# Kernel optimization log

Measured on AMD Instinct MI355X. Metric: run time of the kernel, lower is better.

The kernel has to match this reference:

```python
import jax, jax.numpy as jnp
import numpy as np

NUM_HEADS = 16


def setup_inputs() -> dict:
    key = jax.random.key(0)
    k1, k2, k3 = jax.random.split(key, 3)
    x = jax.random.normal(k1, (2, 2048, 1024), dtype=jnp.float32)
    w_qkv = jax.random.normal(k2, (3072, 1024), dtype=jnp.float32) * 0.02
    b_qkv = jax.random.normal(k3, (3072,), dtype=jnp.float32) * 0.02
    return {"x": x, "w_qkv": w_qkv, "b_qkv": b_qkv}


def reference(x, w_qkv, b_qkv):
    b, s, _ = x.shape
    d_model = w_qkv.shape[0] // 3
    head_dim = d_model // NUM_HEADS
    # fused QKV projection (torch Linear: x @ W^T + b)
    qkv = x @ w_qkv.T + b_qkv                      # [b, s, 3*d_model]
    qkv = qkv.reshape(b, s, NUM_HEADS, 3 * head_dim)
    qkv = jnp.transpose(qkv, (0, 2, 1, 3))          # [b, h, s, 3*hd]
    q, k, v = jnp.split(qkv, 3, axis=-1)            # each [b, h, s, hd]
    scale = 1.0 / np.sqrt(head_dim).astype(np.float32)
    scores = jnp.einsum("bhqd,bhkd->bhqk", q, k) * scale
    attn = jax.nn.softmax(scores, axis=-1)
    values = jnp.einsum("bhqk,bhkd->bhqd", attn, v)  # [b, h, s, hd]
    # Faithful to source: reshape WITHOUT permuting heads back (head-interleaved)
    return values.reshape(b, s, d_model)
```

## Files before the change

### kernel.cpp

```cpp
#include <hip/hip_runtime.h>
#include <cstdint>

typedef unsigned short ushort_t;

#define M_ROWS 4096
#define N_COLS 3072
#define K_DIM  1024
#define S_LEN  2048
#define NHEADS 16
#define HDIM   64
#define QSCALE 0.1803368801111204f

typedef __bf16 bf16_t;
typedef bf16_t  bf16x8  __attribute__((ext_vector_type(8)));
typedef short   shortx4 __attribute__((ext_vector_type(4)));
typedef float   floatx4 __attribute__((ext_vector_type(4)));
typedef ushort_t ushortx4 __attribute__((ext_vector_type(4)));

union U32x2S4 { unsigned u[2]; shortx4 s; };

__device__ __forceinline__ unsigned short f2bf(float f) {
  unsigned u = __float_as_uint(f);
  u += 0x7FFFu + ((u >> 16) & 1u);
  return (unsigned short)(u >> 16);
}

__device__ __forceinline__ unsigned pkbf(float a, float b) {
  unsigned ua = __float_as_uint(a) + 0x8000u;
  unsigned ub = __float_as_uint(b) + 0x8000u;
  return __builtin_amdgcn_perm(ub, ua, 0x07060302u);
}

__device__ __forceinline__ float fexp2(float x) {
#if __has_builtin(__builtin_amdgcn_exp2f)
  return __builtin_amdgcn_exp2f(x);
#else
  float r; asm volatile("v_exp_f32 %0, %1\n\ts_nop 1" : "=v"(r) : "v"(x)); return r;
#endif
}

__device__ __forceinline__ void gload_lds16(const void* g, void* l) {
  __builtin_amdgcn_global_load_lds(
      (const __attribute__((address_space(1))) unsigned int*)g,
      (__attribute__((address_space(3))) unsigned int*)l,
      16, 0, 0);
}

__global__ __launch_bounds__(256) void cvt_bf16_kernel(
    const float* __restrict__ x, const float* __restrict__ w,
    ushort_t* __restrict__ Xb, ushort_t* __restrict__ Wb) {
  const int NX4 = (M_ROWS * K_DIM) / 4;
  int i = blockIdx.x * 256 + threadIdx.x;
  const float4* src;
  ushort_t* dst;
  int idx;
  if (i < NX4) { src = (const float4*)x; dst = Xb; idx = i; }
  else         { src = (const float4*)w; dst = Wb; idx = i - NX4; }
  float4 v = src[idx];
  ushort4 o;
  o.x = f2bf(v.x); o.y = f2bf(v.y); o.z = f2bf(v.z); o.w = f2bf(v.w);
  ((ushort4*)dst)[idx] = o;
}

__global__ __launch_bounds__(256) void qkv_gemm_kernel(
    const ushort_t* __restrict__ Xb, const ushort_t* __restrict__ Wb,
    const float* __restrict__ bias,
    ushort_t* __restrict__ Qb, ushort_t* __restrict__ Kb, ushort_t* __restrict__ Vb) {
  __shared__ ushort_t As[128 * 64];
  __shared__ ushort_t Bs[128 * 64];
  const int tid = threadIdx.x;
  const int l = tid & 63, w = tid >> 6;
  const int quad = l >> 4, lj = l & 15;
  const int m0 = blockIdx.y * 128, n0 = blockIdx.x * 128;
  const int wm = (w & 1) * 64, wn = (w >> 1) * 64;

  floatx4 acc[4][4] = {};

  const int srow = w * 32 + (l >> 3);
  const int scol = ((l & 7) ^ (l >> 3)) * 8;
  const ushort_t* gA = Xb + (size_t)(m0 + srow) * K_DIM + scol;
  const ushort_t* gB = Wb + (size_t)(n0 + srow) * K_DIM + scol;
  ushort_t* lA = As + (w * 32) * 64;
  ushort_t* lB = Bs + (w * 32) * 64;

  const int swr = lj & 7;

  for (int k0 = 0; k0 < K_DIM; k0 += 64) {
    __syncthreads();
#pragma unroll
    for (int c = 0; c < 4; ++c) {
      gload_lds16(gA + (size_t)(c * 8) * K_DIM + k0, lA + c * 8 * 64);
      gload_lds16(gB + (size_t)(c * 8) * K_DIM + k0, lB + c * 8 * 64);
    }
    __syncthreads();
#pragma unroll
    for (int kk = 0; kk < 2; ++kk) {
      const int ch = ((kk * 4 + quad) ^ swr) * 8;
      bf16x8 xF[4], wF[4];
#pragma unroll
      for (int j = 0; j < 4; ++j)
        xF[j] = *(const bf16x8*)(As + (wm + j * 16 + lj) * 64 + ch);
#pragma unroll
      for (int i = 0; i < 4; ++i)
        wF[i] = *(const bf16x8*)(Bs + (wn + i * 16 + lj) * 64 + ch);
#pragma unroll
      for (int i = 0; i < 4; ++i)
#pragma unroll
        for (int j = 0; j < 4; ++j)
          acc[i][j] = __builtin_amdgcn_mfma_f32_16x16x32_bf16(wF[i], xF[j], acc[i][j], 0, 0, 0);
    }
  }

  const int nseg = (n0 + wn) >> 6;
  const int h = nseg / 3;
  const int r = nseg - h * 3;
  ushort_t* dst = (r == 0) ? Qb : (r == 1) ? Kb : Vb;
  const float scl = (r == 0) ? QSCALE : 1.0f;
  const size_t hbase = (size_t)h * S_LEN * HDIM;

#pragma unroll
  for (int i = 0; i < 4; ++i) {
    const int d0 = i * 16 + quad * 4;
    const float4 bv = *(const float4*)(bias + n0 + wn + d0);
#pragma unroll
    for (int j = 0; j < 4; ++j) {
      const float v0 = (acc[i][j][0] + bv.x) * scl;
      const float v1 = (acc[i][j][1] + bv.y) * scl;
      const float v2 = (acc[i][j][2] + bv.z) * scl;
      const float v3 = (acc[i][j][3] + bv.w) * scl;
      uint2 pk;
      pk.x = pkbf(v0, v1);
      pk.y = pkbf(v2, v3);
      const int m = m0 + wm + j * 16 + lj;
      const int bi = m >> 11;
      const int si = m & 2047;
      *(uint2*)(dst + hbase + ((size_t)bi * NHEADS * S_LEN + si) * HDIM + d0) = pk;
    }
  }
}

__global__ __launch_bounds__(512, 4) void attn_kernel(
    const ushort_t* __restrict__ Qb, const ushort_t* __restrict__ Kb,
    const ushort_t* __restrict__ Vb, float* __restrict__ out) {
  __shared__ ushort_t Ks[128 * 64];
  __shared__ ushort_t Vs[64 * 140];
  const int tid = threadIdx.x;
  const int l = tid & 63, w = tid >> 6;
  const int quad = l >> 4, lj = l & 15;
  const int bh = blockIdx.x >> 4;
  const int qt = blockIdx.x & 15;
  const int q0 = qt * 128 + w * 16;
  const size_t headoff = (size_t)bh * S_LEN * HDIM;

  bf16x8 qF[2];
#pragma unroll
  for (int kk = 0; kk < 2; ++kk)
    qF[kk] = *(const bf16x8*)(Qb + headoff + (size_t)(q0 + lj) * HDIM +
                              kk * 32 + quad * 8);

  floatx4 accO[4] = {};
  float l_run = 0.f;

  const int kr = tid >> 3;
  const int kc = ((tid & 7) ^ (kr & 7)) * 8;
  const ushort_t* gK = Kb + headoff + (size_t)kr * HDIM + kc;
  ushort_t* lK = Ks + tid * 8;

  const int dq = tid & 15;
  const int spw = tid >> 4;
  const ushort_t* gV = Vb + headoff + dq * 4;
  unsigned* Vs32 = (unsigned*)Vs;
  const int swz = (dq >> 2) << 1;

  const int swk = lj & 7;

  for (int kb = 0; kb < 16; ++kb) {
    const int kv0 = kb * 128;
    __syncthreads();
#pragma unroll
    for (int c = 0; c < 2; ++c)
      gload_lds16(gK + (size_t)(kv0 + c * 64) * HDIM, lK + c * 64 * 64);
#pragma unroll
    for (int R = 0; R < 2; ++R) {
      const int sp = R * 32 + spw;
      const ushort_t* g = gV + (size_t)(kv0 + 2 * sp) * HDIM;
      const uint2 v0 = *(const uint2*)g;
      const uint2 v1 = *(const uint2*)(g + HDIM);
      unsigned o0 = __builtin_amdgcn_perm(v1.x, v0.x, 0x05040100u);
      unsigned o1 = __builtin_amdgcn_perm(v1.x, v0.x, 0x07060302u);
      unsigned o2 = __builtin_amdgcn_perm(v1.y, v0.y, 0x05040100u);
      unsigned o3 = __builtin_amdgcn_perm(v1.y, v0.y, 0x07060302u);
      const int sp2 = sp ^ swz;
      Vs32[(4 * dq + 0) * 70 + sp2] = o0;
      Vs32[(4 * dq + 1) * 70 + sp2] = o1;
      Vs32[(4 * dq + 2) * 70 + sp2] = o2;
      Vs32[(4 * dq + 3) * 70 + sp2] = o3;
    }
    __syncthreads();

    floatx4 accST[8];
#pragma unroll
    for (int c = 0; c < 8; ++c) {
      const ushort_t* krow = Ks + (c * 16 + lj) * 64;
      bf16x8 kF0 = *(const bf16x8*)(krow + ((quad ^ swk) * 8));
      bf16x8 kF1 = *(const bf16x8*)(krow + (((quad ^ swk) ^ 4) * 8));
      floatx4 z = {0.f, 0.f, 0.f, 0.f};
      z = __builtin_amdgcn_mfma_f32_16x16x32_bf16(kF0, qF[0], z, 0, 0, 0);
      accST[c] = __builtin_amdgcn_mfma_f32_16x16x32_bf16(kF1, qF[1], z, 0, 0, 0);
    }

    shortx4 aP[8];
    float lsum = 0.f;
#pragma unroll
    for (int c = 0; c < 8; ++c) {
      float p0 = fexp2(accST[c][0]);
      float p1 = fexp2(accST[c][1]);
      float p2 = fexp2(accST[c][2]);
      float p3 = fexp2(accST[c][3]);
      lsum += (p0 + p1) + (p2 + p3);
      U32x2S4 t;
      t.u[0] = pkbf(p0, p1);
      t.u[1] = pkbf(p2, p3);
      aP[c] = t.s;
    }
    l_run += lsum;

#pragma unroll
    for (int dt = 0; dt < 4; ++dt) {
      const ushort_t* vp = Vs + (dt * 16 + lj) * 140 + (quad ^ dt) * 4;
#pragma unroll
      for (int c = 0; c < 8; ++c) {
        shortx4 vF = *(const shortx4*)(vp + c * 16);
        accO[dt] = __builtin_amdgcn_mfma_f32_16x16x16bf16_1k(aP[c], vF, accO[dt], 0, 0, 0);
      }
    }
  }

  {
    float ls = l_run;
    ls += __shfl_xor(ls, 16, 64);
    ls += __shfl_xor(ls, 32, 64);
    const float inv = 1.0f / ls;
    const int sbase = (l & 48) | (quad * 4);
    float iv[4];
    iv[0] = __shfl(inv, sbase + 0, 64);
    iv[1] = __shfl(inv, sbase + 1, 64);
    iv[2] = __shfl(inv, sbase + 2, 64);
    iv[3] = __shfl(inv, sbase + 3, 64);
#pragma unroll
    for (int dt = 0; dt < 4; ++dt) {
#pragma unroll
      for (int rg = 0; rg < 4; ++rg) {
        const int q = q0 + quad * 4 + rg;
        out[headoff + (size_t)q * HDIM + dt * 16 + lj] = accO[dt][rg] * iv[rg];
      }
    }
  }
}

extern "C" void kernel_launch(void* const* d_in, const int* in_sizes, int n_in,
                              void* d_out, int out_size, void* d_ws, size_t ws_size,
                              hipStream_t stream) {
  (void)in_sizes; (void)n_in; (void)out_size; (void)ws_size;
  const float* x  = (const float*)d_in[0];
  const float* wq = (const float*)d_in[1];
  const float* bq = (const float*)d_in[2];
  float* out = (float*)d_out;

  char* ws = (char*)d_ws;
  ushort_t* Qb = (ushort_t*)(ws);
  ushort_t* Kb = (ushort_t*)(ws + 8388608);
  ushort_t* Vb = (ushort_t*)(ws + 16777216);
  ushort_t* Xb = (ushort_t*)(ws + 25165824);
  ushort_t* Wb = (ushort_t*)(ws + 33554432);

  cvt_bf16_kernel<<<7168, 256, 0, stream>>>(x, wq, Xb, Wb);
  qkv_gemm_kernel<<<dim3(N_COLS / 128, M_ROWS / 128), 256, 0, stream>>>(Xb, Wb, bq, Qb, Kb, Vb);
  attn_kernel<<<512, 512, 0, stream>>>(Qb, Kb, Vb, out);
}
```

Measured before the change: 171.3 us.

## Switch attention to 32x32 MFMA tiles with four waves per block

The attention kernel now uses 32x32x16 and 32x32x8 bf16 MFMAs, so each wave owns 32 query rows instead of 16. The block drops from 8 waves to 4 with the same 128 queries per block, and each thread loads more of the K/V tile. Processing each 32-key chunk immediately (scores, exp, PV) keeps fewer score registers live. The aim is fewer MFMA issues and fewer LDS fragment reads per FLOP, at the cost of fewer waves to hide latency and new lane-to-row mappings and swizzles that must match exactly.

```diff
diff --git a/kernel.cpp b/kernel.cpp
--- a/kernel.cpp
+++ b/kernel.cpp
@@ -15,6 +15,7 @@
 typedef bf16_t  bf16x8  __attribute__((ext_vector_type(8)));
 typedef short   shortx4 __attribute__((ext_vector_type(4)));
 typedef float   floatx4 __attribute__((ext_vector_type(4)));
+typedef float   floatx16 __attribute__((ext_vector_type(16)));
 typedef ushort_t ushortx4 __attribute__((ext_vector_type(4)));
 
 union U32x2S4 { unsigned u[2]; shortx4 s; };
@@ -139,26 +140,26 @@
   }
 }
 
-__global__ __launch_bounds__(512, 4) void attn_kernel(
+__global__ __launch_bounds__(256, 4) void attn_kernel(
     const ushort_t* __restrict__ Qb, const ushort_t* __restrict__ Kb,
     const ushort_t* __restrict__ Vb, float* __restrict__ out) {
   __shared__ ushort_t Ks[128 * 64];
   __shared__ ushort_t Vs[64 * 140];
   const int tid = threadIdx.x;
   const int l = tid & 63, w = tid >> 6;
-  const int quad = l >> 4, lj = l & 15;
+  const int dl = l & 31, h = l >> 5;
   const int bh = blockIdx.x >> 4;
   const int qt = blockIdx.x & 15;
-  const int q0 = qt * 128 + w * 16;
+  const int q0 = qt * 128 + w * 32;
   const size_t headoff = (size_t)bh * S_LEN * HDIM;
 
-  bf16x8 qF[2];
-#pragma unroll
-  for (int kk = 0; kk < 2; ++kk)
-    qF[kk] = *(const bf16x8*)(Qb + headoff + (size_t)(q0 + lj) * HDIM +
-                              kk * 32 + quad * 8);
-
-  floatx4 accO[4] = {};
+  bf16x8 qF[4];
+#pragma unroll
+  for (int t = 0; t < 4; ++t)
+    qF[t] = *(const bf16x8*)(Qb + headoff + (size_t)(q0 + dl) * HDIM +
+                             t * 16 + h * 8);
+
+  floatx16 accO[2] = {};
   float l_run = 0.f;
 
   const int kr = tid >> 3;
@@ -170,19 +171,17 @@
   const int spw = tid >> 4;
   const ushort_t* gV = Vb + headoff + dq * 4;
   unsigned* Vs32 = (unsigned*)Vs;
-  const int swz = (dq >> 2) << 1;
-
-  const int swk = lj & 7;
+  const int swzw = (dq >> 2) << 1;
 
   for (int kb = 0; kb < 16; ++kb) {
     const int kv0 = kb * 128;
     __syncthreads();
 #pragma unroll
-    for (int c = 0; c < 2; ++c)
-      gload_lds16(gK + (size_t)(kv0 + c * 64) * HDIM, lK + c * 64 * 64);
-#pragma unroll
-    for (int R = 0; R < 2; ++R) {
-      const int sp = R * 32 + spw;
+    for (int c = 0; c < 4; ++c)
+      gload_lds16(gK + (size_t)(kv0 + c * 32) * HDIM, lK + c * 32 * 64);
+#pragma unroll
+    for (int R = 0; R < 4; ++R) {
+      const int sp = R * 16 + spw;
       const ushort_t* g = gV + (size_t)(kv0 + 2 * sp) * HDIM;
       const uint2 v0 = *(const uint2*)g;
       const uint2 v1 = *(const uint2*)(g + HDIM);
@@ -190,7 +189,7 @@
       unsigned o1 = __builtin_amdgcn_perm(v1.x, v0.x, 0x07060302u);
       unsigned o2 = __builtin_amdgcn_perm(v1.y, v0.y, 0x05040100u);
       unsigned o3 = __builtin_amdgcn_perm(v1.y, v0.y, 0x07060302u);
-      const int sp2 = sp ^ swz;
+      const int sp2 = sp ^ swzw;
       Vs32[(4 * dq + 0) * 70 + sp2] = o0;
       Vs32[(4 * dq + 1) * 70 + sp2] = o1;
       Vs32[(4 * dq + 2) * 70 + sp2] = o2;
@@ -198,62 +197,58 @@
     }
     __syncthreads();
 
-    floatx4 accST[8];
-#pragma unroll
-    for (int c = 0; c < 8; ++c) {
-      const ushort_t* krow = Ks + (c * 16 + lj) * 64;
-      bf16x8 kF0 = *(const bf16x8*)(krow + ((quad ^ swk) * 8));
-      bf16x8 kF1 = *(const bf16x8*)(krow + (((quad ^ swk) ^ 4) * 8));
-      floatx4 z = {0.f, 0.f, 0.f, 0.f};
-      z = __builtin_amdgcn_mfma_f32_16x16x32_bf16(kF0, qF[0], z, 0, 0, 0);
-      accST[c] = __builtin_amdgcn_mfma_f32_16x16x32_bf16(kF1, qF[1], z, 0, 0, 0);
-    }
-
-    shortx4 aP[8];
-    float lsum = 0.f;
-#pragma unroll
-    for (int c = 0; c < 8; ++c) {
-      float p0 = fexp2(accST[c][0]);
-      float p1 = fexp2(accST[c][1]);
-      float p2 = fexp2(accST[c][2]);
-      float p3 = fexp2(accST[c][3]);
-      lsum += (p0 + p1) + (p2 + p3);
-      U32x2S4 t;
-      t.u[0] = pkbf(p0, p1);
-      t.u[1] = pkbf(p2, p3);
-      aP[c] = t.s;
-    }
-    l_run += lsum;
-
-#pragma unroll
-    for (int dt = 0; dt < 4; ++dt) {
-      const ushort_t* vp = Vs + (dt * 16 + lj) * 140 + (quad ^ dt) * 4;
-#pragma unroll
-      for (int c = 0; c < 8; ++c) {
-        shortx4 vF = *(const shortx4*)(vp + c * 16);
-        accO[dt] = __builtin_amdgcn_mfma_f32_16x16x16bf16_1k(aP[c], vF, accO[dt], 0, 0, 0);
+#pragma unroll
+    for (int c = 0; c < 4; ++c) {
+      const ushort_t* krow = Ks + (c * 32 + dl) * 64;
+      floatx16 s = {};
+#pragma unroll
+      for (int t = 0; t < 4; ++t) {
+        const int chunk = (t * 2 + h) ^ (dl & 7);
+        bf16x8 kF = *(const bf16x8*)(krow + chunk * 8);
+        s = __builtin_amdgcn_mfma_f32_32x32x16_bf16(kF, qF[t], s, 0, 0, 0);
       }
+
+      shortx4 aPt[4];
+      float lsum = 0.f;
+#pragma unroll
+      for (int c2 = 0; c2 < 4; ++c2) {
+        float p0 = fexp2(s[4 * c2 + 0]);
+        float p1 = fexp2(s[4 * c2 + 1]);
+        float p2 = fexp2(s[4 * c2 + 2]);
+        float p3 = fexp2(s[4 * c2 + 3]);
+        lsum += (p0 + p1) + (p2 + p3);
+        U32x2S4 tpk;
+        tpk.u[0] = pkbf(p0, p1);
+        tpk.u[1] = pkbf(p2, p3);
+        aPt[c2] = tpk.s;
+      }
+      l_run += lsum;
+
+#pragma unroll
+      for (int dt = 0; dt < 2; ++dt) {
+        const int d = dt * 32 + dl;
+        const int rsw = (d >> 4) << 1;
+        const ushort_t* vrow = Vs + d * 140;
+#pragma unroll
+        for (int c2 = 0; c2 < 4; ++c2) {
+          const int col = (c * 16 + c2 * 4 + h * 2) ^ rsw;
+          shortx4 vF = *(const shortx4*)(vrow + 2 * col);
+          accO[dt] = __builtin_amdgcn_mfma_f32_32x32x8bf16_1k(aPt[c2], vF, accO[dt], 0, 0, 0);
+        }
+      }
     }
   }
 
   {
-    float ls = l_run;
-    ls += __shfl_xor(ls, 16, 64);
-    ls += __shfl_xor(ls, 32, 64);
+    float ls = l_run + __shfl_xor(l_run, 32, 64);
     const float inv = 1.0f / ls;
-    const int sbase = (l & 48) | (quad * 4);
-    float iv[4];
-    iv[0] = __shfl(inv, sbase + 0, 64);
-    iv[1] = __shfl(inv, sbase + 1, 64);
-    iv[2] = __shfl(inv, sbase + 2, 64);
-    iv[3] = __shfl(inv, sbase + 3, 64);
-#pragma unroll
-    for (int dt = 0; dt < 4; ++dt) {
-#pragma unroll
-      for (int rg = 0; rg < 4; ++rg) {
-        const int q = q0 + quad * 4 + rg;
-        out[headoff + (size_t)q * HDIM + dt * 16 + lj] = accO[dt][rg] * iv[rg];
-      }
+#pragma unroll
+    for (int r = 0; r < 16; ++r) {
+      const int qloc = (r & 3) + 8 * (r >> 2) + 4 * h;
+      const float iv = __shfl(inv, qloc, 64);
+      float* orow = out + headoff + (size_t)(q0 + qloc) * HDIM + dl;
+      orow[0]  = accO[0][r] * iv;
+      orow[32] = accO[1][r] * iv;
     }
   }
 }
@@ -276,5 +271,5 @@
 
   cvt_bf16_kernel<<<7168, 256, 0, stream>>>(x, wq, Xb, Wb);
   qkv_gemm_kernel<<<dim3(N_COLS / 128, M_ROWS / 128), 256, 0, stream>>>(Xb, Wb, bq, Qb, Kb, Vb);
-  attn_kernel<<<512, 512, 0, stream>>>(Qb, Kb, Vb, out);
-}
+  attn_kernel<<<512, 256, 0, stream>>>(Qb, Kb, Vb, out);
+}
```

Result: slower. 216.5 us (+26.3%).
